# Kernel optimization log

Hardware: AMD Instinct MI355X
Metric: run time of the kernel (lower is better)

## Reference

```python
import jax, jax.numpy as jnp
import numpy as np

DELTA = -5.0
DECAY = 0.95
EPS = 1e-05


def setup_inputs() -> dict:
    key = jax.random.key(0)
    k1, k2, k3 = jax.random.split(key, 3)
    N, K, D = 16384, 1024, 256
    z = jax.random.normal(k1, (N, D), dtype=jnp.float32)
    centroids = jax.random.normal(k2, (K, D), dtype=jnp.float32)
    ema_w = jax.random.normal(k3, (K, D), dtype=jnp.float32)
    ema_cluster_size = jnp.ones((K,), dtype=jnp.float32)
    return {"z": z, "centroids": centroids, "ema_w": ema_w,
            "ema_cluster_size": ema_cluster_size}


def reference(z, centroids, ema_w, ema_cluster_size):
    # z: [N, D]; centroids/ema_w: [K, D]; ema_cluster_size: [K]
    K = centroids.shape[0]
    # squared L2 distances via ||z||^2 - 2 z.C^T + ||c||^2 (same math as
    # sum((z[:,None,:]-C)**2, -1), without the (N,K,D) intermediate)
    z_sq = jnp.sum(z * z, axis=1, keepdims=True)          # [N, 1]
    c_sq = jnp.sum(centroids * centroids, axis=1)         # [K]
    z_dist = z_sq - 2.0 * (z @ centroids.T) + c_sq        # [N, K]
    gamma = jax.nn.softmax(DELTA * z_dist, axis=1)        # [N, K]
    idx = jnp.argmax(gamma, axis=1)                       # [N] int
    # recons = one_hot(idx) @ centroids == gather
    recons = centroids[idx]                               # [N, D]
    # --- EMA codebook update (training branch), expressed purely ---
    counts = jnp.zeros((K,), dtype=z.dtype).at[idx].add(jnp.ones((), z.dtype))
    new_cs = ema_cluster_size * DECAY + (1.0 - DECAY) * counts
    n = jnp.sum(new_cs)
    new_cs = (new_cs + EPS) / (n + K * EPS) * n
    dw = jax.ops.segment_sum(z, idx, num_segments=K)      # == Idx.T @ z, [K, D]
    new_w = ema_w * DECAY + (1.0 - DECAY) * dw
    new_centroids = new_w / new_cs[:, None]
    # straight-through estimator
    recons = z + jax.lax.stop_gradient(recons - z)
    return recons, gamma, new_centroids
```

## Files before the change

### kernel.cpp

```cpp
#include <hip/hip_runtime.h>
#include <hip/hip_bf16.h>


#define DECAY 0.95f
#define OMD   0.05f
#define EPSV  1e-5f

using f32x4  = __attribute__((ext_vector_type(4))) float;
using bf16x8 = __attribute__((ext_vector_type(8))) __bf16;

typedef __attribute__((address_space(3))) unsigned int       lds_uint;
typedef const __attribute__((address_space(1))) unsigned int glb_uint;

__device__ __forceinline__ void gload16(const void* g, const void* l) {
  __builtin_amdgcn_global_load_lds((glb_uint*)(unsigned long long)g,
                                   (lds_uint*)(unsigned int)(unsigned long long)l,
                                   16, 0, 0);
}

__device__ __forceinline__ unsigned short f2bf(float f) {
  unsigned int u = __float_as_uint(f);
  unsigned int r = (u + 0x7FFFu + ((u >> 16) & 1u)) >> 16;
  return (unsigned short)r;
}
__device__ __forceinline__ float bf2f(unsigned short s) {
  return __uint_as_float(((unsigned int)s) << 16);
}

__global__ __launch_bounds__(256) void prep(const float* __restrict__ z,
                                            const float* __restrict__ cent,
                                            const float* __restrict__ ema_cs,
                                            unsigned short* __restrict__ zh,
                                            unsigned short* __restrict__ zl,
                                            unsigned short* __restrict__ chp,
                                            unsigned short* __restrict__ clp,
                                            float* __restrict__ csq,
                                            float* __restrict__ dwzero,
                                            float* __restrict__ S) {
  const int bid = blockIdx.x;
  const int t   = threadIdx.x;
  if (bid < 2048) {
    const int i = bid * 256 + t;
    const float4 a = ((const float4*)z)[2 * i];
    const float4 b = ((const float4*)z)[2 * i + 1];
    float f[8] = {a.x, a.y, a.z, a.w, b.x, b.y, b.z, b.w};
    union { unsigned short u[8]; uint4 v; } H, L;
#pragma unroll
    for (int j = 0; j < 8; ++j) {
      H.u[j] = f2bf(f[j]);
      L.u[j] = f2bf(f[j] - bf2f(H.u[j]));
    }
    ((uint4*)zh)[i] = H.v;
    ((uint4*)zl)[i] = L.v;
  } else if (bid < 2176) {
    const int i = (bid - 2048) * 256 + t;
    const float4 a = ((const float4*)cent)[2 * i];
    const float4 b = ((const float4*)cent)[2 * i + 1];
    float f[8] = {a.x, a.y, a.z, a.w, b.x, b.y, b.z, b.w};
    union { unsigned short u[8]; uint4 v; } H, L;
    float ss = 0.f;
#pragma unroll
    for (int j = 0; j < 8; ++j) {
      H.u[j] = f2bf(f[j]);
      L.u[j] = f2bf(f[j] - bf2f(H.u[j]));
      ss += f[j] * f[j];
    }
    ((uint4*)chp)[i] = H.v;
    ((uint4*)clp)[i] = L.v;
#pragma unroll
    for (int off = 16; off; off >>= 1) ss += __shfl_down(ss, off, 32);
    if ((t & 31) == 0) csq[(bid - 2048) * 8 + (t >> 5)] = ss;
  } else if (bid < 2433) {
    const int i = (bid - 2176) * 256 + t;
    ((float4*)dwzero)[i] = (float4){0.f, 0.f, 0.f, 0.f};
  } else {
    float s = ema_cs[t] + ema_cs[t + 256] + ema_cs[t + 512] + ema_cs[t + 768];
#pragma unroll
    for (int off = 32; off; off >>= 1) s += __shfl_down(s, off);
    __shared__ float wsum[4];
    if ((t & 63) == 0) wsum[t >> 6] = s;
    __syncthreads();
    if (t == 0) S[0] = wsum[0] + wsum[1] + wsum[2] + wsum[3];
  }
}

__global__ __launch_bounds__(256, 2) void dist_gemm_mfma(
    const unsigned short* __restrict__ zh, const unsigned short* __restrict__ zl,
    const unsigned short* __restrict__ ch, const unsigned short* __restrict__ cl,
    const float* __restrict__ csq, float* __restrict__ dist) {
  __shared__ unsigned short lds[4][128 * 64];

  const int tid  = threadIdx.x;
  const int lane = tid & 63;
  const int w    = tid >> 6;

  const int bid = blockIdx.x;
  const int lin = (bid & 7) * 128 + (bid >> 3);
  const int m0  = (lin >> 3) * 128;
  const int n0  = (lin & 7) * 128;

  const int wm0 = (w >> 1) * 64;
  const int wn0 = (w & 1) * 64;

  f32x4 acc[4][4];
#pragma unroll
  for (int i = 0; i < 4; ++i)
#pragma unroll
    for (int j = 0; j < 4; ++j) acc[i][j] = (f32x4){0.f, 0.f, 0.f, 0.f};

  const int srow = lane >> 3;
  const int scb  = lane & 7;

  for (int d0 = 0; d0 < 256; d0 += 64) {
    __syncthreads();
#pragma unroll
    for (int j = 0; j < 4; ++j) {
      const int r0    = w * 32 + j * 8;
      const int row   = r0 + srow;
      const int chunk = scb ^ (row & 7);
      const size_t go = (size_t)(d0 + chunk * 8);
      gload16(zh + (size_t)(m0 + row) * 256 + go, &lds[0][r0 * 64]);
      gload16(zl + (size_t)(m0 + row) * 256 + go, &lds[1][r0 * 64]);
      gload16(ch + (size_t)(n0 + row) * 256 + go, &lds[2][r0 * 64]);
      gload16(cl + (size_t)(n0 + row) * 256 + go, &lds[3][r0 * 64]);
    }
    __syncthreads();
#pragma unroll
    for (int s = 0; s < 2; ++s) {
      bf16x8 ah[4], al[4], bh[4], bl[4];
      const int kg = s * 4 + (lane >> 4);
#pragma unroll
      for (int f = 0; f < 4; ++f) {
        const int ra = wm0 + f * 16 + (lane & 15);
        const int ca = kg ^ (ra & 7);
        ah[f] = *(const bf16x8*)&lds[0][ra * 64 + ca * 8];
        al[f] = *(const bf16x8*)&lds[1][ra * 64 + ca * 8];
        const int rb = wn0 + f * 16 + (lane & 15);
        const int cb = kg ^ (rb & 7);
        bh[f] = *(const bf16x8*)&lds[2][rb * 64 + cb * 8];
        bl[f] = *(const bf16x8*)&lds[3][rb * 64 + cb * 8];
      }
#pragma unroll
      for (int fm = 0; fm < 4; ++fm)
#pragma unroll
        for (int fn = 0; fn < 4; ++fn) {
          acc[fm][fn] = __builtin_amdgcn_mfma_f32_16x16x32_bf16(ah[fm], bh[fn], acc[fm][fn], 0, 0, 0);
          acc[fm][fn] = __builtin_amdgcn_mfma_f32_16x16x32_bf16(ah[fm], bl[fn], acc[fm][fn], 0, 0, 0);
          acc[fm][fn] = __builtin_amdgcn_mfma_f32_16x16x32_bf16(al[fm], bh[fn], acc[fm][fn], 0, 0, 0);
        }
    }
  }

#pragma unroll
  for (int fn = 0; fn < 4; ++fn) {
    const int col = n0 + wn0 + fn * 16 + (lane & 15);
    const float cq = csq[col];
#pragma unroll
    for (int fm = 0; fm < 4; ++fm) {
      const int row = m0 + wm0 + fm * 16 + ((lane >> 4) << 2);
#pragma unroll
      for (int r = 0; r < 4; ++r)
        dist[(size_t)(row + r) * 1024 + col] = cq - 2.0f * acc[fm][fn][r];
    }
  }
}

__global__ __launch_bounds__(256) void row_softmax(const float* __restrict__ z,
                                                   const float* __restrict__ cent,
                                                   float* __restrict__ gamma,
                                                   float* __restrict__ recons,
                                                   float* __restrict__ dw,
                                                   float* __restrict__ counts,
                                                   int K) {
  const int n = blockIdx.x;
  const int t = threadIdx.x;
  float* row = gamma + (size_t)n * K;
  const float4 s = ((const float4*)row)[t];

  float mv = s.x; int mi = 4 * t;
  if (s.y < mv) { mv = s.y; mi = 4 * t + 1; }
  if (s.z < mv) { mv = s.z; mi = 4 * t + 2; }
  if (s.w < mv) { mv = s.w; mi = 4 * t + 3; }

#pragma unroll
  for (int off = 32; off; off >>= 1) {
    const float ov = __shfl_down(mv, off);
    const int   oi = __shfl_down(mi, off);
    if (ov < mv || (ov == mv && oi < mi)) { mv = ov; mi = oi; }
  }

  __shared__ float wv[4];
  __shared__ int   wi[4];
  __shared__ float fmin_s;
  __shared__ int   fidx_s;
  __shared__ float fsum_s;
  const int wave = t >> 6;
  if ((t & 63) == 0) { wv[wave] = mv; wi[wave] = mi; }
  __syncthreads();
  if (t == 0) {
    float bv = wv[0]; int bi = wi[0];
#pragma unroll
    for (int wq = 1; wq < 4; ++wq)
      if (wv[wq] < bv || (wv[wq] == bv && wi[wq] < bi)) { bv = wv[wq]; bi = wi[wq]; }
    fmin_s = bv; fidx_s = bi;
  }
  __syncthreads();

  const float bm = fmin_s;
  const float e0 = __expf(-5.0f * (s.x - bm));
  const float e1 = __expf(-5.0f * (s.y - bm));
  const float e2 = __expf(-5.0f * (s.z - bm));
  const float e3 = __expf(-5.0f * (s.w - bm));
  float ls = e0 + e1 + e2 + e3;
#pragma unroll
  for (int off = 32; off; off >>= 1) ls += __shfl_down(ls, off);
  if ((t & 63) == 0) wv[wave] = ls;
  __syncthreads();
  if (t == 0) fsum_s = wv[0] + wv[1] + wv[2] + wv[3];
  __syncthreads();

  const float inv = 1.0f / fsum_s;
  float4 g;
  g.x = e0 * inv; g.y = e1 * inv; g.z = e2 * inv; g.w = e3 * inv;
  ((float4*)row)[t] = g;

  const int idx = fidx_s;
  const float zv = z[(size_t)n * 256 + t];
  recons[(size_t)n * 256 + t] = cent[(size_t)idx * 256 + t];
  atomicAdd(&dw[(size_t)idx * 256 + t], zv);
  if (t == 0) atomicAdd(&counts[idx], 1.0f);
}

__global__ __launch_bounds__(256) void finalize(const float* __restrict__ ema_w,
                                                const float* __restrict__ ema_cs,
                                                const float* __restrict__ counts,
                                                const float* __restrict__ dw,
                                                const float* __restrict__ S,
                                                float* __restrict__ outc,
                                                float fN) {
  const int k = blockIdx.x;
  const int t = threadIdx.x;
  const float n   = DECAY * S[0] + OMD * fN;
  const float v   = DECAY * ema_cs[k] + OMD * counts[k];
  const float ncs = (v + EPSV) / (n + 1024.0f * EPSV) * n;
  const size_t i  = (size_t)k * 256 + t;
  outc[i] = (DECAY * ema_w[i] + OMD * dw[i]) / ncs;
}

extern "C" void kernel_launch(void* const* d_in, const int* in_sizes, int n_in,
                              void* d_out, int out_size, void* d_ws, size_t ws_size,
                              hipStream_t stream) {
  const float* z      = (const float*)d_in[0];
  const float* cent   = (const float*)d_in[1];
  const float* ema_w  = (const float*)d_in[2];
  const float* ema_cs = (const float*)d_in[3];

  const int K = in_sizes[3];
  const int D = in_sizes[1] / K;
  const int N = in_sizes[0] / D;

  float* out    = (float*)d_out;
  float* recons = out;
  float* gamma  = out + (size_t)N * D;
  float* outc   = gamma + (size_t)N * K;

  unsigned short* zh  = (unsigned short*)recons;
  unsigned short* zl  = zh + (size_t)N * D;
  unsigned short* chp = (unsigned short*)outc;
  unsigned short* clp = chp + (size_t)K * D;

  float* dw     = (float*)d_ws;
  float* counts = dw + (size_t)K * D;
  float* csq    = counts + K;
  float* S      = csq + K;

  prep<<<2434, 256, 0, stream>>>(z, cent, ema_cs, zh, zl, chp, clp, csq, dw, S);

  dist_gemm_mfma<<<(N / 128) * (K / 128), 256, 0, stream>>>(zh, zl, chp, clp, csq, gamma);

  row_softmax<<<N, 256, 0, stream>>>(z, cent, gamma, recons, dw, counts, K);

  finalize<<<K, 256, 0, stream>>>(ema_w, ema_cs, counts, dw, S, outc, (float)N);
}
```

Before: 84.11 us.

## Replace split-bf16 distance GEMM with per-row scaled two-level int8 MFMA

Quantizes z and centroids per row into an int8 high part plus an int8 residual scaled by 256, stored interleaved. The distance GEMM then uses 32x32x32 i8 MFMA with three products (hi*hi, hi*lo, lo*hi) and rescales by the row and column scales in the epilogue. This halves operand bytes and uses the higher int8 matrix throughput in place of the three bf16 MFMAs. It risks precision loss, since the effective mantissa is about 15 bits relative to the row max, and that could flip argmax or shift the softmax values.

```diff
diff --git a/kernel.cpp b/kernel.cpp
--- a/kernel.cpp
+++ b/kernel.cpp
@@ -1,13 +1,12 @@
 #include <hip/hip_runtime.h>
-#include <hip/hip_bf16.h>
 
 
 #define DECAY 0.95f
 #define OMD   0.05f
 #define EPSV  1e-5f
 
-using f32x4  = __attribute__((ext_vector_type(4))) float;
-using bf16x8 = __attribute__((ext_vector_type(8))) __bf16;
+using i32x4  = __attribute__((ext_vector_type(4))) int;
+using i32x16 = __attribute__((ext_vector_type(16))) int;
 
 typedef __attribute__((address_space(3))) unsigned int       lds_uint;
 typedef const __attribute__((address_space(1))) unsigned int glb_uint;
@@ -18,58 +17,56 @@
                                    16, 0, 0);
 }
 
-__device__ __forceinline__ unsigned short f2bf(float f) {
-  unsigned int u = __float_as_uint(f);
-  unsigned int r = (u + 0x7FFFu + ((u >> 16) & 1u)) >> 16;
-  return (unsigned short)r;
-}
-__device__ __forceinline__ float bf2f(unsigned short s) {
-  return __uint_as_float(((unsigned int)s) << 16);
-}
-
 __global__ __launch_bounds__(256) void prep(const float* __restrict__ z,
                                             const float* __restrict__ cent,
                                             const float* __restrict__ ema_cs,
-                                            unsigned short* __restrict__ zh,
-                                            unsigned short* __restrict__ zl,
-                                            unsigned short* __restrict__ chp,
-                                            unsigned short* __restrict__ clp,
+                                            signed char* __restrict__ z8,
+                                            signed char* __restrict__ c8,
+                                            float* __restrict__ sz,
+                                            float* __restrict__ sc,
                                             float* __restrict__ csq,
                                             float* __restrict__ dwzero,
                                             float* __restrict__ S) {
   const int bid = blockIdx.x;
   const int t   = threadIdx.x;
-  if (bid < 2048) {
-    const int i = bid * 256 + t;
-    const float4 a = ((const float4*)z)[2 * i];
-    const float4 b = ((const float4*)z)[2 * i + 1];
+  if (bid < 2176) {
+    const bool isz = bid < 2048;
+    const float* src = isz ? z : cent;
+    const int rb = isz ? bid : (bid - 2048);
+    const int r  = rb * 8 + (t >> 5);
+    const int d0 = (t & 31) * 8;
+    const float4 a = *(const float4*)&src[(size_t)r * 256 + d0];
+    const float4 b = *(const float4*)&src[(size_t)r * 256 + d0 + 4];
     float f[8] = {a.x, a.y, a.z, a.w, b.x, b.y, b.z, b.w};
-    union { unsigned short u[8]; uint4 v; } H, L;
+    float am = 0.f, ssq = 0.f;
+#pragma unroll
+    for (int j = 0; j < 8; ++j) { am = fmaxf(am, fabsf(f[j])); ssq += f[j] * f[j]; }
+#pragma unroll
+    for (int off = 16; off; off >>= 1) {
+      am  = fmaxf(am, __shfl_down(am, off, 32));
+      ssq += __shfl_down(ssq, off, 32);
+    }
+    am = __shfl(am, 0, 32);
+    const float s  = fmaxf(am, 1e-6f) * (1.0f / 127.0f);
+    const float rs = 1.0f / s;
+    union { signed char c[8]; uint2 u; } H, L;
 #pragma unroll
     for (int j = 0; j < 8; ++j) {
-      H.u[j] = f2bf(f[j]);
-      L.u[j] = f2bf(f[j] - bf2f(H.u[j]));
-    }
-    ((uint4*)zh)[i] = H.v;
-    ((uint4*)zl)[i] = L.v;
-  } else if (bid < 2176) {
-    const int i = (bid - 2048) * 256 + t;
-    const float4 a = ((const float4*)cent)[2 * i];
-    const float4 b = ((const float4*)cent)[2 * i + 1];
-    float f[8] = {a.x, a.y, a.z, a.w, b.x, b.y, b.z, b.w};
-    union { unsigned short u[8]; uint4 v; } H, L;
-    float ss = 0.f;
-#pragma unroll
-    for (int j = 0; j < 8; ++j) {
-      H.u[j] = f2bf(f[j]);
-      L.u[j] = f2bf(f[j] - bf2f(H.u[j]));
-      ss += f[j] * f[j];
-    }
-    ((uint4*)chp)[i] = H.v;
-    ((uint4*)clp)[i] = L.v;
-#pragma unroll
-    for (int off = 16; off; off >>= 1) ss += __shfl_down(ss, off, 32);
-    if ((t & 31) == 0) csq[(bid - 2048) * 8 + (t >> 5)] = ss;
+      float q = rintf(f[j] * rs);
+      q = fminf(fmaxf(q, -127.f), 127.f);
+      H.c[j] = (signed char)(int)q;
+      float res = f[j] - q * s;
+      float lq = rintf(res * rs * 256.0f);
+      lq = fminf(fmaxf(lq, -127.f), 127.f);
+      L.c[j] = (signed char)(int)lq;
+    }
+    signed char* dst = (isz ? z8 : c8) + (size_t)r * 512 + (d0 >> 6) * 128 + (d0 & 63);
+    *(uint2*)dst        = H.u;
+    *(uint2*)(dst + 64) = L.u;
+    if ((t & 31) == 0) {
+      if (isz) sz[r] = s;
+      else { sc[r] = s; csq[r] = ssq; }
+    }
   } else if (bid < 2433) {
     const int i = (bid - 2176) * 256 + t;
     ((float4*)dwzero)[i] = (float4){0.f, 0.f, 0.f, 0.f};
@@ -84,11 +81,11 @@
   }
 }
 
-__global__ __launch_bounds__(256, 2) void dist_gemm_mfma(
-    const unsigned short* __restrict__ zh, const unsigned short* __restrict__ zl,
-    const unsigned short* __restrict__ ch, const unsigned short* __restrict__ cl,
+__global__ __launch_bounds__(256, 2) void dist_gemm_i8(
+    const signed char* __restrict__ z8, const signed char* __restrict__ c8,
+    const float* __restrict__ sz, const float* __restrict__ sc,
     const float* __restrict__ csq, float* __restrict__ dist) {
-  __shared__ unsigned short lds[4][128 * 64];
+  __shared__ signed char lds[2][128 * 128];
 
   const int tid  = threadIdx.x;
   const int lane = tid & 63;
@@ -102,65 +99,67 @@
   const int wm0 = (w >> 1) * 64;
   const int wn0 = (w & 1) * 64;
 
-  f32x4 acc[4][4];
-#pragma unroll
-  for (int i = 0; i < 4; ++i)
-#pragma unroll
-    for (int j = 0; j < 4; ++j) acc[i][j] = (f32x4){0.f, 0.f, 0.f, 0.f};
+  i32x16 accA[2][2];
+  i32x16 accB[2][2];
+#pragma unroll
+  for (int i = 0; i < 2; ++i)
+#pragma unroll
+    for (int j = 0; j < 2; ++j) {
+      accA[i][j] = (i32x16)(0);
+      accB[i][j] = (i32x16)(0);
+    }
 
   const int srow = lane >> 3;
   const int scb  = lane & 7;
 
-  for (int d0 = 0; d0 < 256; d0 += 64) {
+  for (int kk = 0; kk < 4; ++kk) {
     __syncthreads();
 #pragma unroll
     for (int j = 0; j < 4; ++j) {
       const int r0    = w * 32 + j * 8;
       const int row   = r0 + srow;
       const int chunk = scb ^ (row & 7);
-      const size_t go = (size_t)(d0 + chunk * 8);
-      gload16(zh + (size_t)(m0 + row) * 256 + go, &lds[0][r0 * 64]);
-      gload16(zl + (size_t)(m0 + row) * 256 + go, &lds[1][r0 * 64]);
-      gload16(ch + (size_t)(n0 + row) * 256 + go, &lds[2][r0 * 64]);
-      gload16(cl + (size_t)(n0 + row) * 256 + go, &lds[3][r0 * 64]);
+      gload16(z8 + (size_t)(m0 + row) * 512 + kk * 128 + chunk * 16, &lds[0][r0 * 128]);
+      gload16(c8 + (size_t)(n0 + row) * 512 + kk * 128 + chunk * 16, &lds[1][r0 * 128]);
     }
     __syncthreads();
 #pragma unroll
     for (int s = 0; s < 2; ++s) {
-      bf16x8 ah[4], al[4], bh[4], bl[4];
-      const int kg = s * 4 + (lane >> 4);
-#pragma unroll
-      for (int f = 0; f < 4; ++f) {
-        const int ra = wm0 + f * 16 + (lane & 15);
-        const int ca = kg ^ (ra & 7);
-        ah[f] = *(const bf16x8*)&lds[0][ra * 64 + ca * 8];
-        al[f] = *(const bf16x8*)&lds[1][ra * 64 + ca * 8];
-        const int rb = wn0 + f * 16 + (lane & 15);
-        const int cb = kg ^ (rb & 7);
-        bh[f] = *(const bf16x8*)&lds[2][rb * 64 + cb * 8];
-        bl[f] = *(const bf16x8*)&lds[3][rb * 64 + cb * 8];
+      i32x4 ah[2], al[2], bh[2], bl[2];
+      const int kc = s * 2 + (lane >> 5);
+#pragma unroll
+      for (int fi = 0; fi < 2; ++fi) {
+        const int ra = wm0 + fi * 32 + (lane & 31);
+        ah[fi] = *(const i32x4*)&lds[0][ra * 128 + ((kc)     ^ (ra & 7)) * 16];
+        al[fi] = *(const i32x4*)&lds[0][ra * 128 + ((kc + 4) ^ (ra & 7)) * 16];
+        const int rb = wn0 + fi * 32 + (lane & 31);
+        bh[fi] = *(const i32x4*)&lds[1][rb * 128 + ((kc)     ^ (rb & 7)) * 16];
+        bl[fi] = *(const i32x4*)&lds[1][rb * 128 + ((kc + 4) ^ (rb & 7)) * 16];
       }
 #pragma unroll
-      for (int fm = 0; fm < 4; ++fm)
-#pragma unroll
-        for (int fn = 0; fn < 4; ++fn) {
-          acc[fm][fn] = __builtin_amdgcn_mfma_f32_16x16x32_bf16(ah[fm], bh[fn], acc[fm][fn], 0, 0, 0);
-          acc[fm][fn] = __builtin_amdgcn_mfma_f32_16x16x32_bf16(ah[fm], bl[fn], acc[fm][fn], 0, 0, 0);
-          acc[fm][fn] = __builtin_amdgcn_mfma_f32_16x16x32_bf16(al[fm], bh[fn], acc[fm][fn], 0, 0, 0);
+      for (int i = 0; i < 2; ++i)
+#pragma unroll
+        for (int j = 0; j < 2; ++j) {
+          accA[i][j] = __builtin_amdgcn_mfma_i32_32x32x32_i8(ah[i], bh[j], accA[i][j], 0, 0, 0);
+          accB[i][j] = __builtin_amdgcn_mfma_i32_32x32x32_i8(ah[i], bl[j], accB[i][j], 0, 0, 0);
+          accB[i][j] = __builtin_amdgcn_mfma_i32_32x32x32_i8(al[i], bh[j], accB[i][j], 0, 0, 0);
         }
     }
   }
 
 #pragma unroll
-  for (int fn = 0; fn < 4; ++fn) {
-    const int col = n0 + wn0 + fn * 16 + (lane & 15);
-    const float cq = csq[col];
-#pragma unroll
-    for (int fm = 0; fm < 4; ++fm) {
-      const int row = m0 + wm0 + fm * 16 + ((lane >> 4) << 2);
-#pragma unroll
-      for (int r = 0; r < 4; ++r)
-        dist[(size_t)(row + r) * 1024 + col] = cq - 2.0f * acc[fm][fn][r];
+  for (int j = 0; j < 2; ++j) {
+    const int colb = n0 + wn0 + j * 32 + (lane & 31);
+    const float scv = sc[colb];
+    const float cqv = csq[colb];
+#pragma unroll
+    for (int i = 0; i < 2; ++i) {
+#pragma unroll
+      for (int reg = 0; reg < 16; ++reg) {
+        const int row = m0 + wm0 + i * 32 + (reg & 3) + 8 * (reg >> 2) + 4 * (lane >> 5);
+        const float dotv = (float)accA[i][j][reg] + (float)accB[i][j][reg] * (1.0f / 256.0f);
+        dist[(size_t)row * 1024 + colb] = cqv - 2.0f * sz[row] * scv * dotv;
+      }
     }
   }
 }
@@ -264,19 +263,19 @@
   float* gamma  = out + (size_t)N * D;
   float* outc   = gamma + (size_t)N * K;
 
-  unsigned short* zh  = (unsigned short*)recons;
-  unsigned short* zl  = zh + (size_t)N * D;
-  unsigned short* chp = (unsigned short*)outc;
-  unsigned short* clp = chp + (size_t)K * D;
+  signed char* z8 = (signed char*)recons;
+  signed char* c8 = (signed char*)outc;
+  float* sz = outc + (size_t)K * 512 / 4;
+  float* sc = sz + N;
 
   float* dw     = (float*)d_ws;
   float* counts = dw + (size_t)K * D;
   float* csq    = counts + K;
   float* S      = csq + K;
 
-  prep<<<2434, 256, 0, stream>>>(z, cent, ema_cs, zh, zl, chp, clp, csq, dw, S);
-
-  dist_gemm_mfma<<<(N / 128) * (K / 128), 256, 0, stream>>>(zh, zl, chp, clp, csq, gamma);
+  prep<<<2434, 256, 0, stream>>>(z, cent, ema_cs, z8, c8, sz, sc, csq, dw, S);
+
+  dist_gemm_i8<<<(N / 128) * (K / 128), 256, 0, stream>>>(z8, c8, sz, sc, csq, gamma);
 
   row_softmax<<<N, 256, 0, stream>>>(z, cent, gamma, recons, dw, counts, K);
 
```

New measurement: 77.67 us. 1.08x faster.
